# Kernel optimization log

Measured on AMD Instinct MI355X. Metric: run time of the kernel, lower is better.

Reference implementation:

```python
import jax, jax.numpy as jnp
import numpy as np

N = 10000       # nodes
E = 320000      # random edges (self-loops added separately)
IN_SIZE = 2
UNITS = 64
B = 32


def setup_inputs() -> dict:
    # --- build normalized Laplacian edges (matches calculate_laplacian) ---
    rng = np.random.default_rng(0)
    rows = np.concatenate([rng.integers(0, N, E), np.arange(N)]).astype(np.int32)
    cols = np.concatenate([rng.integers(0, N, E), np.arange(N)]).astype(np.int32)
    vals = np.ones(E + N, dtype=np.float32)  # A + I entries
    rowsum = np.zeros(N, dtype=np.float64)
    np.add.at(rowsum, rows, vals.astype(np.float64))
    d = np.where(rowsum > 0, rowsum ** -0.5, 0.0).astype(np.float32)
    # normalized_adj: M = D^-1/2 A^T D^-1/2  ->  M[c, r] = d[r]*d[c]*A[r, c]
    m_rows = jnp.asarray(cols, dtype=jnp.int32)
    m_cols = jnp.asarray(rows, dtype=jnp.int32)
    m_vals = jnp.asarray(vals * d[rows] * d[cols])

    key = jax.random.key(0)
    k = jax.random.split(key, 6)
    F = UNITS + IN_SIZE
    stdv1 = 1.0 / np.sqrt(2 * UNITS)
    stdv2 = 1.0 / np.sqrt(UNITS)
    w1 = jax.random.uniform(k[0], (F, 2 * UNITS), jnp.float32, -stdv1, stdv1)
    b1 = jax.random.uniform(k[1], (2 * UNITS,), jnp.float32, -stdv1, stdv1)
    w2 = jax.random.uniform(k[2], (F, UNITS), jnp.float32, -stdv2, stdv2)
    b2 = jax.random.uniform(k[3], (UNITS,), jnp.float32, -stdv2, stdv2)
    inputs = jax.random.normal(k[4], (B, N * IN_SIZE), jnp.float32)
    state = jax.random.normal(k[5], (B, N * UNITS), jnp.float32)
    return {"inputs": inputs, "state": state, "m_rows": m_rows, "m_cols": m_cols,
            "m_vals": m_vals, "w1": w1, "b1": b1, "w2": w2, "b2": b2}


def _gc(inputs, state, m_rows, m_cols, m_vals, w, b, out_size):
    # [B, N, F] with F = in_size + units
    x_s = jnp.concatenate(
        [inputs.reshape(B, N, IN_SIZE), state.reshape(B, N, UNITS)], axis=2)
    f = x_s.shape[2]
    x0 = jnp.transpose(x_s, (1, 2, 0)).reshape(N, f * B)  # einsum ijk->jki, flatten
    # sparse spmm: x1 = M @ x0
    x1 = jax.ops.segment_sum(m_vals[:, None] * x0[m_cols], m_rows, num_segments=N)
    x = jnp.transpose(x1.reshape(N, f, B), (2, 0, 1)).reshape(B * N, f)  # ijk->kij
    x = x @ w + b
    return x.reshape(B, N * out_size)


def reference(inputs, state, m_rows, m_cols, m_vals, w1, b1, w2, b2):
    value = jax.nn.sigmoid(_gc(inputs, state, m_rows, m_cols, m_vals, w1, b1, 2 * UNITS))
    # NOTE: faithful to original: split of FLATTENED [B, N*2U] at the midpoint
    r, u = jnp.split(value, 2, axis=1)
    c = jax.nn.relu(_gc(inputs, r * state, m_rows, m_cols, m_vals, w2, b2, UNITS))
    new_h = u * state + (1.0 - u) * c
    return new_h
```

## Files before the change

### kernel.cpp

```cpp
#include <hip/hip_runtime.h>
#include <hip/hip_fp16.h>
#include <cstdint>
#include <cstdio>

#define N_NODES 10000
#define BATCH   32
#define UNITS   64
#define F_DIM   66
#define XROW    2048
#define MAXE    128
#define KPAD    96
#define ASTR    104

typedef float v2f __attribute__((ext_vector_type(2)));
typedef float f32x4 __attribute__((ext_vector_type(4)));
typedef _Float16 half8 __attribute__((ext_vector_type(8)));

__device__ __forceinline__ float sigmoidf(float x) {
  return 1.0f / (1.0f + __expf(-x));
}

__global__ __launch_bounds__(256) void hist_k(const int* __restrict__ rows,
                                              int* __restrict__ counts, int E2) {
  int e = blockIdx.x * 256 + threadIdx.x;
  if (e < E2) atomicAdd(&counts[rows[e]], 1);
}

__global__ __launch_bounds__(256) void scan_k(const int* __restrict__ counts,
                                              int* __restrict__ rowptr,
                                              int* __restrict__ wofs, int n) {
  __shared__ int lbuf[10240];
  __shared__ int sums[256];
  int t = threadIdx.x;
  for (int i = t; i < N_NODES / 4; i += 256)
    reinterpret_cast<int4*>(lbuf)[i] = reinterpret_cast<const int4*>(counts)[i];
  for (int i = N_NODES + t; i < 10240; i += 256) lbuf[i] = 0;
  __syncthreads();
  int base = t * 40;
  int v[40];
  int run = 0;
#pragma unroll
  for (int i = 0; i < 40; ++i) { v[i] = run; run += lbuf[base + i]; }
  sums[t] = run;
  __syncthreads();
  for (int off = 1; off < 256; off <<= 1) {
    int x = (t >= off) ? sums[t - off] : 0;
    __syncthreads();
    sums[t] += x;
    __syncthreads();
  }
  int tbase = (t == 0) ? 0 : sums[t - 1];
#pragma unroll
  for (int i = 0; i < 40; ++i) lbuf[base + i] = tbase + v[i];
  __syncthreads();
  for (int i = t; i < N_NODES / 4; i += 256) {
    int4 w = reinterpret_cast<int4*>(lbuf)[i];
    reinterpret_cast<int4*>(rowptr)[i] = w;
    reinterpret_cast<int4*>(wofs)[i] = w;
  }
  if (t == 255) rowptr[N_NODES] = sums[255];
}

__global__ __launch_bounds__(256) void scatter_k(const int* __restrict__ rows,
                                                 const int* __restrict__ cols,
                                                 const float* __restrict__ vals,
                                                 int* __restrict__ wofs,
                                                 int* __restrict__ ccol,
                                                 float* __restrict__ cval, int E2) {
  int e = blockIdx.x * 256 + threadIdx.x;
  if (e < E2) {
    int r = rows[e];
    int p = atomicAdd(&wofs[r], 1);
    ccol[p] = cols[e] << 11;
    cval[p] = vals[e];
  }
}

__global__ __launch_bounds__(256) void prep_w(const float* __restrict__ w1,
                                              const float* __restrict__ w2,
                                              _Float16* __restrict__ w1T,
                                              _Float16* __restrict__ w2T) {
  int i = blockIdx.x * 256 + threadIdx.x;
  if (i < 128 * KPAD) {
    int j = i / KPAD, f = i % KPAD;
    w1T[i] = (f < 66) ? (_Float16)w1[f * 128 + j] : (_Float16)0.0f;
  } else if (i < 128 * KPAD + 64 * KPAD) {
    int k = i - 128 * KPAD;
    int j = k / KPAD, f = k % KPAD;
    w2T[k] = (f < 66) ? (_Float16)w2[f * 64 + j] : (_Float16)0.0f;
  }
}

__device__ __forceinline__ void pack_row_fp8(const float* T, int n, int t,
                                             unsigned char* xcat8) {
  int k0 = t * 8;
  int f8 = k0 >> 5;
  int b0 = k0 & 31;
  const float* Ts = &T[(f8 + 2) * 33 + b0];
  int d0 = __builtin_amdgcn_cvt_pk_fp8_f32(Ts[0], Ts[1], 0, false);
  d0     = __builtin_amdgcn_cvt_pk_fp8_f32(Ts[2], Ts[3], d0, true);
  int d1 = __builtin_amdgcn_cvt_pk_fp8_f32(Ts[4], Ts[5], 0, false);
  d1     = __builtin_amdgcn_cvt_pk_fp8_f32(Ts[6], Ts[7], d1, true);
  *reinterpret_cast<uint2*>(xcat8 + (size_t)n * XROW + k0) = make_uint2(d0, d1);
}

__global__ __launch_bounds__(256) void build_x1(const float* __restrict__ inputs,
                                                const float* __restrict__ state,
                                                unsigned char* __restrict__ xcat8,
                                                __half2* __restrict__ xin) {
  int n = blockIdx.x, t = threadIdx.x;
  __shared__ float T[66 * 33];
  int f = t & 63, bq = t >> 6;
#pragma unroll
  for (int bb = 0; bb < 8; ++bb) {
    int b = bq + bb * 4;
    T[(f + 2) * 33 + b] = state[(size_t)b * 640000 + (size_t)n * 64 + f];
  }
  if (t < 64) {
    int b0 = t & 31, f0 = t >> 5;
    T[f0 * 33 + b0] = inputs[(size_t)b0 * 20000 + (size_t)n * 2 + f0];
  }
  __syncthreads();
  pack_row_fp8(T, n, t, xcat8);
  if (t < 32) {
    int f0 = t >> 4, b = (t & 15) * 2;
    xin[(size_t)n * 32 + t] = __floats2half2_rn(T[f0 * 33 + b], T[f0 * 33 + b + 1]);
  }
}

__global__ __launch_bounds__(256) void yin_k(const int* __restrict__ rowptr,
                                             const int* __restrict__ ccol,
                                             const float* __restrict__ cval,
                                             const __half* __restrict__ xin,
                                             float* __restrict__ yin) {
  int n = blockIdx.x * 32 + (threadIdx.x >> 3);
  int lane = threadIdx.x & 7;
  if (n >= N_NODES) return;
  float acc[8];
#pragma unroll
  for (int i = 0; i < 8; ++i) acc[i] = 0.0f;
  int s = rowptr[n], e = rowptr[n + 1];
  for (int ee = s; ee < e; ++ee) {
    int c = ccol[ee];
    float v = cval[ee];
    const char* p = reinterpret_cast<const char*>(xin) + (size_t)(unsigned)(c >> 4);
    uint4 raw = reinterpret_cast<const uint4*>(p)[lane];
    const __half2* h = reinterpret_cast<const __half2*>(&raw);
#pragma unroll
    for (int i = 0; i < 4; ++i) {
      float2 x = __half22float2(h[i]);
      acc[2 * i]     += v * x.x;
      acc[2 * i + 1] += v * x.y;
    }
  }
  float4* dst = reinterpret_cast<float4*>(yin + (size_t)n * 64 + lane * 8);
  dst[0] = make_float4(acc[0], acc[1], acc[2], acc[3]);
  dst[1] = make_float4(acc[4], acc[5], acc[6], acc[7]);
}

__device__ __forceinline__ void consume8f8(uint2 u, float v, v2f* acc) {
  v2f p0 = __builtin_amdgcn_cvt_pk_f32_fp8((int)u.x, false);
  v2f p1 = __builtin_amdgcn_cvt_pk_f32_fp8((int)u.x, true);
  v2f p2 = __builtin_amdgcn_cvt_pk_f32_fp8((int)u.y, false);
  v2f p3 = __builtin_amdgcn_cvt_pk_f32_fp8((int)u.y, true);
  v2f vv = {v, v};
  acc[0] += vv * p0;
  acc[1] += vv * p1;
  acc[2] += vv * p2;
  acc[3] += vv * p3;
}

#define LDE(RR, VV, IDX) do { int2 cv = eCV[(IDX)]; \
  RR = *reinterpret_cast<const uint2*>(xbase + (size_t)(unsigned)cv.x); \
  VV = __int_as_float(cv.y); } while (0)

__device__ __forceinline__ void spmm_body(int n, int t,
                                          const int* __restrict__ rowptr,
                                          const int* __restrict__ ccol,
                                          const float* __restrict__ cval,
                                          const unsigned char* __restrict__ xcat8,
                                          const float* __restrict__ yin,
                                          _Float16* accH, int2* eCV) {
  v2f acc[4];
#pragma unroll
  for (int i = 0; i < 4; ++i) acc[i] = (v2f){0.0f, 0.0f};

  const char* xbase = reinterpret_cast<const char*>(xcat8) + (size_t)t * 8;

  int s = rowptr[n], e = rowptr[n + 1];
  for (int cs = s; cs < e; cs += MAXE) {
    int cnt = min(e - cs, MAXE);
    __syncthreads();
    for (int i = t; i < cnt; i += 256) {
      eCV[i] = make_int2(ccol[cs + i], __float_as_int(cval[cs + i]));
    }
    __syncthreads();

    uint2 r0 = {0,0}, r1 = {0,0}, r2 = {0,0}, r3 = {0,0}, r4 = {0,0}, r5 = {0,0}, r6 = {0,0};
    float v0 = 0, v1 = 0, v2 = 0, v3 = 0, v4 = 0, v5 = 0, v6 = 0;
    if (cnt > 0) LDE(r0, v0, 0);
    if (cnt > 1) LDE(r1, v1, 1);
    if (cnt > 2) LDE(r2, v2, 2);
    if (cnt > 3) LDE(r3, v3, 3);
    if (cnt > 4) LDE(r4, v4, 4);
    if (cnt > 5) LDE(r5, v5, 5);
    if (cnt > 6) LDE(r6, v6, 6);
    int j = 0;
    for (; j + 13 < cnt; j += 7) {
      consume8f8(r0, v0, acc); LDE(r0, v0, j + 7);
      consume8f8(r1, v1, acc); LDE(r1, v1, j + 8);
      consume8f8(r2, v2, acc); LDE(r2, v2, j + 9);
      consume8f8(r3, v3, acc); LDE(r3, v3, j + 10);
      consume8f8(r4, v4, acc); LDE(r4, v4, j + 11);
      consume8f8(r5, v5, acc); LDE(r5, v5, j + 12);
      consume8f8(r6, v6, acc); LDE(r6, v6, j + 13);
    }
    for (; j + 7 < cnt; ++j) {
      consume8f8(r0, v0, acc);
      uint2 nr; float nv;
      LDE(nr, nv, j + 7);
      r0 = r1; v0 = v1; r1 = r2; v1 = v2; r2 = r3; v2 = v3;
      r3 = r4; v3 = v4; r4 = r5; v4 = v5; r5 = r6; v5 = v6;
      r6 = nr; v6 = nv;
    }
    if (j + 0 < cnt) consume8f8(r0, v0, acc);
    if (j + 1 < cnt) consume8f8(r1, v1, acc);
    if (j + 2 < cnt) consume8f8(r2, v2, acc);
    if (j + 3 < cnt) consume8f8(r3, v3, acc);
    if (j + 4 < cnt) consume8f8(r4, v4, acc);
    if (j + 5 < cnt) consume8f8(r5, v5, acc);
    if (j + 6 < cnt) consume8f8(r6, v6, acc);
  }

  {
    int f8 = t >> 2;
    int b0 = (t & 3) * 8;
    float a[8] = {acc[0].x, acc[0].y, acc[1].x, acc[1].y,
                  acc[2].x, acc[2].y, acc[3].x, acc[3].y};
    _Float16* dst = accH + (f8 + 2);
#pragma unroll
    for (int i = 0; i < 8; ++i) {
      dst[(b0 + i) * ASTR] = (_Float16)a[i];
    }
  }
  if (t < 64) {
    int f = t >> 5, b = t & 31;
    accH[b * ASTR + f] = (_Float16)yin[(size_t)n * 64 + t];
  }
  for (int id = t; id < 32 * 19; id += 256) {
    int b = id / 19, c = id % 19;
    *reinterpret_cast<unsigned int*>(
        reinterpret_cast<char*>(accH) + b * (ASTR * 2) + 132 + c * 4) = 0u;
  }
  __syncthreads();
}

__global__ __launch_bounds__(256) void gcn1(const int* __restrict__ rowptr,
                                            const int* __restrict__ ccol,
                                            const float* __restrict__ cval,
                                            const unsigned char* __restrict__ xcat8,
                                            const float* __restrict__ yin,
                                            const _Float16* __restrict__ w1T,
                                            const float* __restrict__ b1,
                                            const float* __restrict__ state,
                                            unsigned char* __restrict__ xcat2,
                                            __half* __restrict__ valu) {
  int n = blockIdx.x, t = threadIdx.x;
  __shared__ _Float16 accH[32 * ASTR];
  __shared__ int2  eCV[MAXE];
  __shared__ __align__(16) char regionA[32 * 136 * 2];

  spmm_body(n, t, rowptr, ccol, cval, xcat8, yin, accH, eCV);

  int wv = t >> 6, l = t & 63;
  int mt = wv & 1, ntb = (wv >> 1) * 4;
  int lr = l & 15, lg = l >> 4;
  const _Float16* aB = accH + (size_t)(mt * 16 + lr) * ASTR + lg * 8;
  half8 afr0 = *reinterpret_cast<const half8*>(aB);
  half8 afr1 = *reinterpret_cast<const half8*>(aB + 32);
  half8 afr2 = *reinterpret_cast<const half8*>(aB + 64);
  _Float16* vstage = reinterpret_cast<_Float16*>(regionA);

#pragma unroll
  for (int tt = 0; tt < 4; ++tt) {
    int j = (ntb + tt) * 16 + lr;
    const _Float16* wB = w1T + (size_t)j * KPAD + lg * 8;
    f32x4 c = {0.0f, 0.0f, 0.0f, 0.0f};
    c = __builtin_amdgcn_mfma_f32_16x16x32_f16(afr0, *reinterpret_cast<const half8*>(wB), c, 0, 0, 0);
    c = __builtin_amdgcn_mfma_f32_16x16x32_f16(afr1, *reinterpret_cast<const half8*>(wB + 32), c, 0, 0, 0);
    c = __builtin_amdgcn_mfma_f32_16x16x32_f16(afr2, *reinterpret_cast<const half8*>(wB + 64), c, 0, 0, 0);
    float bj = b1[j];
#pragma unroll
    for (int i = 0; i < 4; ++i) {
      int b = mt * 16 + lg * 4 + i;
      vstage[b * 136 + j] = (_Float16)sigmoidf(c[i] + bj);
    }
  }
  __syncthreads();

  if (n < 5000) {
    int nn_i = t >> 7, rem = t & 127;
    int f = rem >> 1, b0 = (rem & 1) * 16;
    int nn = n * 2 + nn_i;
    int jj = nn_i * 64 + f;
    const float* sp = state + (size_t)b0 * 640000 + (size_t)nn * 64 + f;
    const _Float16* vp = vstage + b0 * 136 + jj;
    unsigned int d[4];
#pragma unroll
    for (int q = 0; q < 4; ++q) {
      float x0 = (float)vp[(4 * q + 0) * 136] * sp[(size_t)(4 * q + 0) * 640000];
      float x1 = (float)vp[(4 * q + 1) * 136] * sp[(size_t)(4 * q + 1) * 640000];
      float x2 = (float)vp[(4 * q + 2) * 136] * sp[(size_t)(4 * q + 2) * 640000];
      float x3 = (float)vp[(4 * q + 3) * 136] * sp[(size_t)(4 * q + 3) * 640000];
      int dd = __builtin_amdgcn_cvt_pk_fp8_f32(x0, x1, 0, false);
      dd     = __builtin_amdgcn_cvt_pk_fp8_f32(x2, x3, dd, true);
      d[q] = (unsigned)dd;
    }
    *reinterpret_cast<uint4*>(xcat2 + (size_t)nn * XROW + f * 32 + b0) =
        make_uint4(d[0], d[1], d[2], d[3]);
  } else {
    int b = t >> 3, jg = t & 7;
    const uint4* src = reinterpret_cast<const uint4*>(vstage + b * 136 + jg * 16);
    uint4 q0 = src[0];
    uint4 q1 = src[1];
    __half* vb = valu + (size_t)(n - 5000) * 4096 + b * 128 + jg * 16;
    *reinterpret_cast<uint4*>(vb) = q0;
    *reinterpret_cast<uint4*>(vb + 8) = q1;
  }
}

__global__ __launch_bounds__(256) void gcn2(const int* __restrict__ rowptr,
                                            const int* __restrict__ ccol,
                                            const float* __restrict__ cval,
                                            const unsigned char* __restrict__ xcat2,
                                            const float* __restrict__ yin,
                                            const _Float16* __restrict__ w2T,
                                            const float* __restrict__ b2,
                                            const __half* __restrict__ valu,
                                            const float* __restrict__ state,
                                            float* __restrict__ out) {
  int n = blockIdx.x, t = threadIdx.x;
  __shared__ _Float16 accH[32 * ASTR];
  __shared__ int2  eCV[MAXE];
  __shared__ __align__(16) char regionA[32 * 68 * 4];

  spmm_body(n, t, rowptr, ccol, cval, xcat2, yin, accH, eCV);

  int wv = t >> 6, l = t & 63;
  int mt = wv & 1, ntb = (wv >> 1) * 2;
  int lr = l & 15, lg = l >> 4;
  const _Float16* aB = accH + (size_t)(mt * 16 + lr) * ASTR + lg * 8;
  half8 afr0 = *reinterpret_cast<const half8*>(aB);
  half8 afr1 = *reinterpret_cast<const half8*>(aB + 32);
  half8 afr2 = *reinterpret_cast<const half8*>(aB + 64);
  float* ostage = reinterpret_cast<float*>(regionA);

#pragma unroll
  for (int tt = 0; tt < 2; ++tt) {
    int j = (ntb + tt) * 16 + lr;
    const _Float16* wB = w2T + (size_t)j * KPAD + lg * 8;
    f32x4 c = {0.0f, 0.0f, 0.0f, 0.0f};
    c = __builtin_amdgcn_mfma_f32_16x16x32_f16(afr0, *reinterpret_cast<const half8*>(wB), c, 0, 0, 0);
    c = __builtin_amdgcn_mfma_f32_16x16x32_f16(afr1, *reinterpret_cast<const half8*>(wB + 32), c, 0, 0, 0);
    c = __builtin_amdgcn_mfma_f32_16x16x32_f16(afr2, *reinterpret_cast<const half8*>(wB + 64), c, 0, 0, 0);
    float bj = b2[j];
#pragma unroll
    for (int i = 0; i < 4; ++i) {
      int b = mt * 16 + lg * 4 + i;
      ostage[b * 68 + j] = fmaxf(c[i] + bj, 0.0f);
    }
  }
  __syncthreads();

  int bg = t >> 4, jg = t & 15;
  int n2 = n >> 1, no = n & 1;
  const __half* up = valu + (size_t)n2 * 4096 + (size_t)no * 64 + jg * 4;
#pragma unroll
  for (int i = 0; i < 2; ++i) {
    int b = bg * 2 + i;
    size_t idx = (size_t)b * 640000 + (size_t)n * 64 + jg * 4;
    float4 sv = *reinterpret_cast<const float4*>(state + idx);
    float4 cc = *reinterpret_cast<const float4*>(ostage + b * 68 + jg * 4);
    union { uint2 u; __half2 h[2]; } pk;
    pk.u = *reinterpret_cast<const uint2*>(up + (size_t)b * 128);
    float2 u01 = __half22float2(pk.h[0]);
    float2 u23 = __half22float2(pk.h[1]);
    float4 h;
    h.x = u01.x * sv.x + (1.0f - u01.x) * cc.x;
    h.y = u01.y * sv.y + (1.0f - u01.y) * cc.y;
    h.z = u23.x * sv.z + (1.0f - u23.x) * cc.z;
    h.w = u23.y * sv.w + (1.0f - u23.y) * cc.w;
    *reinterpret_cast<float4*>(out + idx) = h;
  }
}

static inline size_t alignup(size_t x) { return (x + 255) & ~(size_t)255; }

extern "C" void kernel_launch(void* const* d_in, const int* in_sizes, int n_in,
                              void* d_out, int out_size, void* d_ws, size_t ws_size,
                              hipStream_t stream) {
  const float* inputs = (const float*)d_in[0];
  const float* state  = (const float*)d_in[1];
  const int*   m_rows = (const int*)d_in[2];
  const int*   m_cols = (const int*)d_in[3];
  const float* m_vals = (const float*)d_in[4];
  const float* w1     = (const float*)d_in[5];
  const float* b1     = (const float*)d_in[6];
  const float* w2     = (const float*)d_in[7];
  const float* b2     = (const float*)d_in[8];
  float* out = (float*)d_out;

  const int N  = N_NODES;
  const int E2 = in_sizes[2];

  char* ws = (char*)d_ws;
  size_t off = 0;
  int* counts = (int*)(ws + off); off = alignup(off + (size_t)N * 4);
  int* rowptr = (int*)(ws + off); off = alignup(off + (size_t)(N + 1) * 4);
  int* wofs   = (int*)(ws + off); off = alignup(off + (size_t)N * 4);
  int* ccol   = (int*)(ws + off); off = alignup(off + (size_t)E2 * 4);
  float* cval = (float*)(ws + off); off = alignup(off + (size_t)E2 * 4);
  unsigned char* xcat8 = (unsigned char*)(ws + off); off = alignup(off + (size_t)N * XROW);
  unsigned char* xcat2 = (unsigned char*)(ws + off); off = alignup(off + (size_t)N * XROW);
  __half* valu = (__half*)(ws + off); off = alignup(off + (size_t)5000 * 4096 * 2);
  float* yin  = (float*)(ws + off); off = alignup(off + (size_t)N * 64 * 4);
  __half* xin = (__half*)(ws + off); off = alignup(off + (size_t)N * 64 * 2);
  _Float16* w1T = (_Float16*)(ws + off); off = alignup(off + (size_t)128 * KPAD * 2);
  _Float16* w2T = (_Float16*)(ws + off); off = alignup(off + (size_t)64 * KPAD * 2);
  if (off > ws_size) { return; }

  hipMemsetAsync(counts, 0, (size_t)N * 4, stream);

  int eb = (E2 + 255) / 256;
  int wb = (128 * KPAD + 64 * KPAD + 255) / 256;
  hipLaunchKernelGGL(hist_k,    dim3(eb), dim3(256), 0, stream, m_rows, counts, E2);
  hipLaunchKernelGGL(scan_k,    dim3(1),  dim3(256), 0, stream, counts, rowptr, wofs, N);
  hipLaunchKernelGGL(scatter_k, dim3(eb), dim3(256), 0, stream, m_rows, m_cols, m_vals,
                     wofs, ccol, cval, E2);
  hipLaunchKernelGGL(prep_w,    dim3(wb), dim3(256), 0, stream, w1, w2, w1T, w2T);
  hipLaunchKernelGGL(build_x1,  dim3(N),  dim3(256), 0, stream, inputs, state, xcat8,
                     (__half2*)xin);
  hipLaunchKernelGGL(yin_k,     dim3((N + 31) / 32), dim3(256), 0, stream,
                     rowptr, ccol, cval, xin, yin);
  hipLaunchKernelGGL(gcn1,      dim3(N),  dim3(256), 0, stream, rowptr, ccol, cval,
                     xcat8, yin, w1T, b1, state, xcat2, valu);
  hipLaunchKernelGGL(gcn2,      dim3(N),  dim3(256), 0, stream, rowptr, ccol, cval,
                     xcat2, yin, w2T, b2, valu, state, out);
}
```

Before: 452.1 us.

## Pack edge col/val into int2, drop LDS staging, double-buffer gathers in groups of eight

The scatter kernel now writes each edge's column and value as one interleaved int2 array, so the SpMM kernels read edge metadata straight from global memory instead of staging 128-edge chunks in shared memory behind two __syncthreads per chunk. The gather loop is restructured into groups of eight edges with two register buffers that alternate, padding the tail with zero-valued entries. The weight-transpose prep is folded into the histogram kernel, removing one launch. The trade-off is that every thread issues redundant global loads of the edge metadata and the pipeline holds more registers in flight.

```diff
diff --git a/kernel.cpp b/kernel.cpp
--- a/kernel.cpp
+++ b/kernel.cpp
@@ -8,7 +8,6 @@
 #define UNITS   64
 #define F_DIM   66
 #define XROW    2048
-#define MAXE    128
 #define KPAD    96
 #define ASTR    104
 
@@ -21,9 +20,21 @@
 }
 
 __global__ __launch_bounds__(256) void hist_k(const int* __restrict__ rows,
-                                              int* __restrict__ counts, int E2) {
+                                              int* __restrict__ counts, int E2,
+                                              const float* __restrict__ w1,
+                                              const float* __restrict__ w2,
+                                              _Float16* __restrict__ w1T,
+                                              _Float16* __restrict__ w2T) {
   int e = blockIdx.x * 256 + threadIdx.x;
   if (e < E2) atomicAdd(&counts[rows[e]], 1);
+  if (e < 128 * KPAD) {
+    int j = e / KPAD, f = e % KPAD;
+    w1T[e] = (f < 66) ? (_Float16)w1[f * 128 + j] : (_Float16)0.0f;
+  } else if (e < 128 * KPAD + 64 * KPAD) {
+    int k = e - 128 * KPAD;
+    int j = k / KPAD, f = k % KPAD;
+    w2T[k] = (f < 66) ? (_Float16)w2[f * 64 + j] : (_Float16)0.0f;
+  }
 }
 
 __global__ __launch_bounds__(256) void scan_k(const int* __restrict__ counts,
@@ -65,29 +76,12 @@
                                                  const int* __restrict__ cols,
                                                  const float* __restrict__ vals,
                                                  int* __restrict__ wofs,
-                                                 int* __restrict__ ccol,
-                                                 float* __restrict__ cval, int E2) {
+                                                 int2* __restrict__ ecv, int E2) {
   int e = blockIdx.x * 256 + threadIdx.x;
   if (e < E2) {
     int r = rows[e];
     int p = atomicAdd(&wofs[r], 1);
-    ccol[p] = cols[e] << 11;
-    cval[p] = vals[e];
-  }
-}
-
-__global__ __launch_bounds__(256) void prep_w(const float* __restrict__ w1,
-                                              const float* __restrict__ w2,
-                                              _Float16* __restrict__ w1T,
-                                              _Float16* __restrict__ w2T) {
-  int i = blockIdx.x * 256 + threadIdx.x;
-  if (i < 128 * KPAD) {
-    int j = i / KPAD, f = i % KPAD;
-    w1T[i] = (f < 66) ? (_Float16)w1[f * 128 + j] : (_Float16)0.0f;
-  } else if (i < 128 * KPAD + 64 * KPAD) {
-    int k = i - 128 * KPAD;
-    int j = k / KPAD, f = k % KPAD;
-    w2T[k] = (f < 66) ? (_Float16)w2[f * 64 + j] : (_Float16)0.0f;
+    ecv[p] = make_int2(cols[e] << 11, __float_as_int(vals[e]));
   }
 }
 
@@ -129,8 +123,7 @@
 }
 
 __global__ __launch_bounds__(256) void yin_k(const int* __restrict__ rowptr,
-                                             const int* __restrict__ ccol,
-                                             const float* __restrict__ cval,
+                                             const int2* __restrict__ ecv,
                                              const __half* __restrict__ xin,
                                              float* __restrict__ yin) {
   int n = blockIdx.x * 32 + (threadIdx.x >> 3);
@@ -141,9 +134,9 @@
   for (int i = 0; i < 8; ++i) acc[i] = 0.0f;
   int s = rowptr[n], e = rowptr[n + 1];
   for (int ee = s; ee < e; ++ee) {
-    int c = ccol[ee];
-    float v = cval[ee];
-    const char* p = reinterpret_cast<const char*>(xin) + (size_t)(unsigned)(c >> 4);
+    int2 cv = ecv[ee];
+    float v = __int_as_float(cv.y);
+    const char* p = reinterpret_cast<const char*>(xin) + (size_t)((unsigned)cv.x >> 4);
     uint4 raw = reinterpret_cast<const uint4*>(p)[lane];
     const __half2* h = reinterpret_cast<const __half2*>(&raw);
 #pragma unroll
@@ -170,66 +163,56 @@
   acc[3] += vv * p3;
 }
 
-#define LDE(RR, VV, IDX) do { int2 cv = eCV[(IDX)]; \
-  RR = *reinterpret_cast<const uint2*>(xbase + (size_t)(unsigned)cv.x); \
-  VV = __int_as_float(cv.y); } while (0)
+__device__ __forceinline__ void ld_grp(const int2* __restrict__ ep, int gsz,
+                                       const unsigned char* __restrict__ xcat8,
+                                       unsigned t8, uint2* r, float* v) {
+#pragma unroll
+  for (int q = 0; q < 8; ++q) {
+    int2 c = ep[q];
+    if (q >= gsz) { c.x = 0; c.y = 0; }
+    unsigned off = (unsigned)c.x + t8;
+    r[q] = *reinterpret_cast<const uint2*>(xcat8 + off);
+    v[q] = __int_as_float(c.y);
+  }
+}
+
+__device__ __forceinline__ void cons_grp(const uint2* r, const float* v, v2f* acc) {
+#pragma unroll
+  for (int q = 0; q < 8; ++q) consume8f8(r[q], v[q], acc);
+}
 
 __device__ __forceinline__ void spmm_body(int n, int t,
                                           const int* __restrict__ rowptr,
-                                          const int* __restrict__ ccol,
-                                          const float* __restrict__ cval,
+                                          const int2* __restrict__ ecv,
                                           const unsigned char* __restrict__ xcat8,
                                           const float* __restrict__ yin,
-                                          _Float16* accH, int2* eCV) {
+                                          _Float16* accH) {
   v2f acc[4];
 #pragma unroll
   for (int i = 0; i < 4; ++i) acc[i] = (v2f){0.0f, 0.0f};
 
-  const char* xbase = reinterpret_cast<const char*>(xcat8) + (size_t)t * 8;
-
+  unsigned t8 = (unsigned)t * 8u;
   int s = rowptr[n], e = rowptr[n + 1];
-  for (int cs = s; cs < e; cs += MAXE) {
-    int cnt = min(e - cs, MAXE);
-    __syncthreads();
-    for (int i = t; i < cnt; i += 256) {
-      eCV[i] = make_int2(ccol[cs + i], __float_as_int(cval[cs + i]));
-    }
-    __syncthreads();
-
-    uint2 r0 = {0,0}, r1 = {0,0}, r2 = {0,0}, r3 = {0,0}, r4 = {0,0}, r5 = {0,0}, r6 = {0,0};
-    float v0 = 0, v1 = 0, v2 = 0, v3 = 0, v4 = 0, v5 = 0, v6 = 0;
-    if (cnt > 0) LDE(r0, v0, 0);
-    if (cnt > 1) LDE(r1, v1, 1);
-    if (cnt > 2) LDE(r2, v2, 2);
-    if (cnt > 3) LDE(r3, v3, 3);
-    if (cnt > 4) LDE(r4, v4, 4);
-    if (cnt > 5) LDE(r5, v5, 5);
-    if (cnt > 6) LDE(r6, v6, 6);
-    int j = 0;
-    for (; j + 13 < cnt; j += 7) {
-      consume8f8(r0, v0, acc); LDE(r0, v0, j + 7);
-      consume8f8(r1, v1, acc); LDE(r1, v1, j + 8);
-      consume8f8(r2, v2, acc); LDE(r2, v2, j + 9);
-      consume8f8(r3, v3, acc); LDE(r3, v3, j + 10);
-      consume8f8(r4, v4, acc); LDE(r4, v4, j + 11);
-      consume8f8(r5, v5, acc); LDE(r5, v5, j + 12);
-      consume8f8(r6, v6, acc); LDE(r6, v6, j + 13);
-    }
-    for (; j + 7 < cnt; ++j) {
-      consume8f8(r0, v0, acc);
-      uint2 nr; float nv;
-      LDE(nr, nv, j + 7);
-      r0 = r1; v0 = v1; r1 = r2; v1 = v2; r2 = r3; v2 = v3;
-      r3 = r4; v3 = v4; r4 = r5; v4 = v5; r5 = r6; v5 = v6;
-      r6 = nr; v6 = nv;
-    }
-    if (j + 0 < cnt) consume8f8(r0, v0, acc);
-    if (j + 1 < cnt) consume8f8(r1, v1, acc);
-    if (j + 2 < cnt) consume8f8(r2, v2, acc);
-    if (j + 3 < cnt) consume8f8(r3, v3, acc);
-    if (j + 4 < cnt) consume8f8(r4, v4, acc);
-    if (j + 5 < cnt) consume8f8(r5, v5, acc);
-    if (j + 6 < cnt) consume8f8(r6, v6, acc);
+  int ne = e - s;
+  int ng = (ne + 7) >> 3;
+  const int2* ep = ecv + s;
+
+  uint2 rA[8], rB[8];
+  float vA[8], vB[8];
+  ld_grp(ep, ne, xcat8, t8, rA, vA);
+  int g = 1;
+  for (; g + 1 < ng; g += 2) {
+    ld_grp(ep + 8 * g, ne - 8 * g, xcat8, t8, rB, vB);
+    cons_grp(rA, vA, acc);
+    ld_grp(ep + 8 * (g + 1), ne - 8 * (g + 1), xcat8, t8, rA, vA);
+    cons_grp(rB, vB, acc);
+  }
+  if (g < ng) {
+    ld_grp(ep + 8 * g, ne - 8 * g, xcat8, t8, rB, vB);
+    cons_grp(rA, vA, acc);
+    cons_grp(rB, vB, acc);
+  } else {
+    cons_grp(rA, vA, acc);
   }
 
   {
@@ -256,8 +239,7 @@
 }
 
 __global__ __launch_bounds__(256) void gcn1(const int* __restrict__ rowptr,
-                                            const int* __restrict__ ccol,
-                                            const float* __restrict__ cval,
+                                            const int2* __restrict__ ecv,
                                             const unsigned char* __restrict__ xcat8,
                                             const float* __restrict__ yin,
                                             const _Float16* __restrict__ w1T,
@@ -267,10 +249,9 @@
                                             __half* __restrict__ valu) {
   int n = blockIdx.x, t = threadIdx.x;
   __shared__ _Float16 accH[32 * ASTR];
-  __shared__ int2  eCV[MAXE];
   __shared__ __align__(16) char regionA[32 * 136 * 2];
 
-  spmm_body(n, t, rowptr, ccol, cval, xcat8, yin, accH, eCV);
+  spmm_body(n, t, rowptr, ecv, xcat8, yin, accH);
 
   int wv = t >> 6, l = t & 63;
   int mt = wv & 1, ntb = (wv >> 1) * 4;
@@ -330,8 +311,7 @@
 }
 
 __global__ __launch_bounds__(256) void gcn2(const int* __restrict__ rowptr,
-                                            const int* __restrict__ ccol,
-                                            const float* __restrict__ cval,
+                                            const int2* __restrict__ ecv,
                                             const unsigned char* __restrict__ xcat2,
                                             const float* __restrict__ yin,
                                             const _Float16* __restrict__ w2T,
@@ -341,10 +321,9 @@
                                             float* __restrict__ out) {
   int n = blockIdx.x, t = threadIdx.x;
   __shared__ _Float16 accH[32 * ASTR];
-  __shared__ int2  eCV[MAXE];
   __shared__ __align__(16) char regionA[32 * 68 * 4];
 
-  spmm_body(n, t, rowptr, ccol, cval, xcat2, yin, accH, eCV);
+  spmm_body(n, t, rowptr, ecv, xcat2, yin, accH);
 
   int wv = t >> 6, l = t & 63;
   int mt = wv & 1, ntb = (wv >> 1) * 2;
@@ -418,8 +397,7 @@
   int* counts = (int*)(ws + off); off = alignup(off + (size_t)N * 4);
   int* rowptr = (int*)(ws + off); off = alignup(off + (size_t)(N + 1) * 4);
   int* wofs   = (int*)(ws + off); off = alignup(off + (size_t)N * 4);
-  int* ccol   = (int*)(ws + off); off = alignup(off + (size_t)E2 * 4);
-  float* cval = (float*)(ws + off); off = alignup(off + (size_t)E2 * 4);
+  int2* ecv   = (int2*)(ws + off); off = alignup(off + (size_t)E2 * 8 + 64);
   unsigned char* xcat8 = (unsigned char*)(ws + off); off = alignup(off + (size_t)N * XROW);
   unsigned char* xcat2 = (unsigned char*)(ws + off); off = alignup(off + (size_t)N * XROW);
   __half* valu = (__half*)(ws + off); off = alignup(off + (size_t)5000 * 4096 * 2);
@@ -432,18 +410,17 @@
   hipMemsetAsync(counts, 0, (size_t)N * 4, stream);
 
   int eb = (E2 + 255) / 256;
-  int wb = (128 * KPAD + 64 * KPAD + 255) / 256;
-  hipLaunchKernelGGL(hist_k,    dim3(eb), dim3(256), 0, stream, m_rows, counts, E2);
+  hipLaunchKernelGGL(hist_k,    dim3(eb), dim3(256), 0, stream, m_rows, counts, E2,
+                     w1, w2, w1T, w2T);
   hipLaunchKernelGGL(scan_k,    dim3(1),  dim3(256), 0, stream, counts, rowptr, wofs, N);
   hipLaunchKernelGGL(scatter_k, dim3(eb), dim3(256), 0, stream, m_rows, m_cols, m_vals,
-                     wofs, ccol, cval, E2);
-  hipLaunchKernelGGL(prep_w,    dim3(wb), dim3(256), 0, stream, w1, w2, w1T, w2T);
+                     wofs, ecv, E2);
   hipLaunchKernelGGL(build_x1,  dim3(N),  dim3(256), 0, stream, inputs, state, xcat8,
                      (__half2*)xin);
   hipLaunchKernelGGL(yin_k,     dim3((N + 31) / 32), dim3(256), 0, stream,
-                     rowptr, ccol, cval, xin, yin);
-  hipLaunchKernelGGL(gcn1,      dim3(N),  dim3(256), 0, stream, rowptr, ccol, cval,
+                     rowptr, ecv, xin, yin);
+  hipLaunchKernelGGL(gcn1,      dim3(N),  dim3(256), 0, stream, rowptr, ecv,
                      xcat8, yin, w1T, b1, state, xcat2, valu);
-  hipLaunchKernelGGL(gcn2,      dim3(N),  dim3(256), 0, stream, rowptr, ccol, cval,
+  hipLaunchKernelGGL(gcn2,      dim3(N),  dim3(256), 0, stream, rowptr, ecv,
                      xcat2, yin, w2T, b2, valu, state, out);
 }
```

Result: faster. 438.9 us (-2.9%).
